# Kernel tuning notes

Hardware: AMD Instinct MI355X
Metric: run time of the kernel (lower is better)

The kernel has to match this reference:

```python
import jax, jax.numpy as jnp
import numpy as np

D_IN, D_SAE, T, L, K = 2304, 2048, 4, 6, 128
B = 32


def setup_inputs() -> dict:
    key = jax.random.key(0)
    kx, ke, kd = jax.random.split(key, 3)
    x = jax.random.normal(kx, (B, T, L, D_IN), dtype=jnp.float32)
    W_enc = jax.random.normal(ke, (T, L, D_IN, D_SAE), dtype=jnp.float32) / np.sqrt(D_IN).astype(np.float32)
    W_dec = jax.random.normal(kd, (T, L, D_SAE, D_IN), dtype=jnp.float32) / np.sqrt(D_SAE).astype(np.float32)
    b_enc = jnp.zeros((D_SAE,), dtype=jnp.float32)
    b_dec = jnp.zeros((T, L, D_IN), dtype=jnp.float32)
    return {"x": x, "W_enc": W_enc, "W_dec": W_dec, "b_enc": b_enc, "b_dec": b_dec}


def reference(x, W_enc, W_dec, b_enc, b_dec):
    # encode: per-(t,l) matmul, pre: (B, T, L, d_sae)
    pre = jnp.einsum('btld,tlds->btls', x, W_enc) + b_enc
    Bn = pre.shape[0]
    pre_flat = pre.reshape(Bn, T * L * D_SAE)
    # global TopK over the whole (T, L, d_sae) latent grid
    v, idx = jax.lax.top_k(pre_flat, K)
    z_flat = jnp.zeros_like(pre_flat).at[jnp.arange(Bn)[:, None], idx].set(jax.nn.relu(v))
    z = z_flat.reshape(Bn, T, L, D_SAE)
    # decode: per-(t,l) matmul
    x_hat = jnp.einsum('btls,tlsd->btld', z, W_dec) + b_dec
    loss = jnp.mean(jnp.sum(jnp.square(x_hat - x), axis=-1))
    return (loss, x_hat, z)
```

## Files before the change

### kernel.cpp

```cpp
#include <hip/hip_runtime.h>

#define D_IN   2304
#define D_SAE  2048
#define TL     24
#define BATCH  32
#define K_TOP  128
#define NLAT   (TL * D_SAE)
#define NBIN   8192
#define CAP    2048
#define KSPLIT 4
#define KS     (D_IN / KSPLIT)
#define BK     16
#define NCH    (KS / BK)

__device__ __forceinline__ void async_cp16(const float* g, float* l) {
    __builtin_amdgcn_global_load_lds(
        (const __attribute__((address_space(1))) unsigned int*)g,
        (__attribute__((address_space(3))) unsigned int*)l, 16, 0, 0);
}

__global__ __launch_bounds__(256, 3) void enc_kernel(const float* __restrict__ x,
                                                     const float* __restrict__ W,
                                                     float* __restrict__ part) {
    __shared__ float w_s[2][BK][256];
    __shared__ float x_s[2][BATCH][BK];

    const int tid  = threadIdx.x;
    const int lane = tid & 63;
    const int wv   = tid >> 6;
    const int cg   = tid & 63;
    const int tl   = blockIdx.y;
    const int ks   = blockIdx.z;

    const float* Wbase = W + ((size_t)(tl * D_IN + ks * KS)) * D_SAE + blockIdx.x * 256;

#define STAGE(buf, ch)                                                          \
    do {                                                                        \
        const float* Wc = Wbase + (size_t)((ch) * BK) * D_SAE;                  \
        _Pragma("unroll")                                                       \
        for (int j = 0; j < 4; ++j)                                             \
            async_cp16(Wc + (size_t)(wv * 4 + j) * D_SAE + lane * 4,            \
                       &w_s[buf][wv * 4 + j][0]);                               \
        _Pragma("unroll")                                                       \
        for (int p = 0; p < 2; ++p) {                                           \
            int f = p * 256 + lane * 4;      \
            int xb = f >> 4, xk = f & 15;                                       \
            async_cp16(x + ((size_t)(xb * TL + tl)) * D_IN + ks * KS            \
                         + (ch) * BK + xk,                                      \
                       &x_s[buf][0][0] + p * 256);                              \
        }                                                                       \
    } while (0)

    float4 acc[8];
#pragma unroll
    for (int j = 0; j < 8; ++j) acc[j] = make_float4(0.f, 0.f, 0.f, 0.f);

    STAGE(0, 0);

    int cur = 0;
    for (int ch = 0; ch < NCH; ++ch) {
        if (ch + 1 < NCH) {
            STAGE(cur ^ 1, ch + 1);
            asm volatile("s_waitcnt vmcnt(6)" ::: "memory");
        } else {
            asm volatile("s_waitcnt vmcnt(0)" ::: "memory");
        }
        asm volatile("s_barrier" ::: "memory");

        const float(*ws)[256] = w_s[cur];
        const float(*xs)[BK]  = x_s[cur];
#pragma unroll
        for (int k = 0; k < BK; ++k) {
            float4 w4 = *(const float4*)&ws[k][cg * 4];
#pragma unroll
            for (int j = 0; j < 8; ++j) {
                float xv = xs[wv * 8 + j][k];
                acc[j].x = fmaf(xv, w4.x, acc[j].x);
                acc[j].y = fmaf(xv, w4.y, acc[j].y);
                acc[j].z = fmaf(xv, w4.z, acc[j].z);
                acc[j].w = fmaf(xv, w4.w, acc[j].w);
            }
        }
        asm volatile("s_barrier" ::: "memory");
        cur ^= 1;
    }
#undef STAGE

    float* pp = part + ((size_t)ks * BATCH + wv * 8) * NLAT
              + (size_t)tl * D_SAE + blockIdx.x * 256 + cg * 4;
#pragma unroll
    for (int j = 0; j < 8; ++j)
        *(float4*)&pp[(size_t)j * NLAT] = acc[j];
}

__global__ void reduce_kernel(const float* __restrict__ part,
                              const float* __restrict__ b_enc,
                              float* __restrict__ pre) {
    int i = (blockIdx.x * blockDim.x + threadIdx.x) * 4;
    const size_t S = (size_t)BATCH * NLAT;
    float4 v = *(const float4*)&part[i];
    float4 v1 = *(const float4*)&part[i + S];
    float4 v2 = *(const float4*)&part[i + 2 * S];
    float4 v3 = *(const float4*)&part[i + 3 * S];
    float4 bb = *(const float4*)&b_enc[i & (D_SAE - 1)];
    v.x += v1.x + v2.x + v3.x + bb.x;
    v.y += v1.y + v2.y + v3.y + bb.y;
    v.z += v1.z + v2.z + v3.z + bb.z;
    v.w += v1.w + v2.w + v3.w + bb.w;
    *(float4*)&pre[i] = v;
}

__global__ __launch_bounds__(256) void topk_kernel(const float* __restrict__ pre,
                                                   int* __restrict__ sel_idx,
                                                   float* __restrict__ sel_val,
                                                   float* __restrict__ z,
                                                   float* __restrict__ loss) {
    const int b   = blockIdx.x;
    const int tid = threadIdx.x;
    __shared__ unsigned hist[NBIN];
    __shared__ unsigned cand_key[CAP];
    __shared__ int      cand_idx[CAP];
    __shared__ unsigned tsum[256];
    __shared__ unsigned suf[256];
    __shared__ int s_T, s_hi, s_ccnt, s_sel;

    const float* row  = pre + (size_t)b * NLAT;
    float*       zrow = z   + (size_t)b * NLAT;
    for (int i = tid; i < NBIN; i += 256) hist[i] = 0;
    if (tid == 0) { s_ccnt = 0; s_sel = 0; if (b == 0) *loss = 0.f; }
    __syncthreads();

    for (int i = 4 * tid; i < NLAT; i += 1024) {
        float4 v = *(const float4*)&row[i];
#pragma unroll
        for (int j = 0; j < 4; j++) {
            unsigned u   = __float_as_uint(((const float*)&v)[j]);
            unsigned key = u ^ ((u >> 31) ? 0xFFFFFFFFu : 0x80000000u);
            atomicAdd(&hist[key >> 19], 1u);
        }
    }
    __syncthreads();

    unsigned local = 0;
    const int base = tid * (NBIN / 256);
    for (int j = 0; j < NBIN / 256; j++) local += hist[base + j];
    tsum[tid] = local;
    __syncthreads();
    if (tid == 0) {
        unsigned run = 0;
        for (int t = 255; t >= 0; t--) { suf[t] = run; run += tsum[t]; }
    }
    __syncthreads();
    if (suf[tid] < K_TOP && suf[tid] + tsum[tid] >= K_TOP) {
        unsigned c = suf[tid];
        for (int j = NBIN / 256 - 1; j >= 0; j--) {
            int bin = base + j;
            if (c + hist[bin] >= K_TOP) { s_T = bin; s_hi = (int)c; break; }
            c += hist[bin];
        }
    }
    __syncthreads();

    const int T = s_T;
    for (int i = 4 * tid; i < NLAT; i += 1024) {
        float4 v = *(const float4*)&row[i];
#pragma unroll
        for (int j = 0; j < 4; j++) {
            float f      = ((const float*)&v)[j];
            unsigned u   = __float_as_uint(f);
            unsigned key = u ^ ((u >> 31) ? 0xFFFFFFFFu : 0x80000000u);
            int bin      = (int)(key >> 19);
            float rl     = fmaxf(f, 0.f);
            float zval   = 0.f;
            if (bin > T) {
                int p = atomicAdd(&s_sel, 1);
                sel_idx[b * K_TOP + p] = i + j;
                sel_val[b * K_TOP + p] = rl;
                zval = rl;
            } else if (bin == T) {
                int p = atomicAdd(&s_ccnt, 1);
                if (p < CAP) { cand_key[p] = key; cand_idx[p] = i + j; }
            }
            zrow[i + j] = zval;
        }
    }
    __syncthreads();

    const int need = K_TOP - s_hi;
    const int nc   = min(s_ccnt, CAP);
    for (int c = tid; c < nc; c += 256) {
        unsigned kc = cand_key[c]; int ic = cand_idx[c];
        int rank = 0;
        for (int j = 0; j < nc; j++) {
            unsigned kj = cand_key[j]; int ij = cand_idx[j];
            rank += (kj > kc) || (kj == kc && ij < ic);
        }
        if (rank < need) {
            int p = atomicAdd(&s_sel, 1);
            float rl = fmaxf(row[ic], 0.f);
            sel_idx[b * K_TOP + p] = ic;
            sel_val[b * K_TOP + p] = rl;
            zrow[ic] = rl;
        }
    }
}

__global__ __launch_bounds__(256) void dec_kernel(const float* __restrict__ Wd,
                                                  const float* __restrict__ b_dec,
                                                  const float* __restrict__ x,
                                                  const int* __restrict__ sel_idx,
                                                  const float* __restrict__ sel_val,
                                                  float* __restrict__ xhat,
                                                  float* __restrict__ loss) {
    const int tl = blockIdx.x, b = blockIdx.y, tid = threadIdx.x;
    float acc[9];
#pragma unroll
    for (int r = 0; r < 9; r++) acc[r] = b_dec[tl * D_IN + tid + r * 256];

    __shared__ int   s_idx[K_TOP];
    __shared__ float s_val[K_TOP];
    if (tid < K_TOP) { s_idx[tid] = sel_idx[b * K_TOP + tid];
                       s_val[tid] = sel_val[b * K_TOP + tid]; }
    __syncthreads();

    for (int j = 0; j < K_TOP; j++) {
        int f = s_idx[j];
        if ((f >> 11) == tl) {
            float v = s_val[j];
            const float* wrow = Wd + (size_t)f * D_IN;
#pragma unroll
            for (int r = 0; r < 9; r++)
                acc[r] = fmaf(v, wrow[tid + r * 256], acc[r]);
        }
    }

    const float* xr = x    + ((size_t)b * TL + tl) * D_IN;
    float*       xo = xhat + ((size_t)b * TL + tl) * D_IN;
    float lsum = 0.f;
#pragma unroll
    for (int r = 0; r < 9; r++) {
        float d = acc[r] - xr[tid + r * 256];
        xo[tid + r * 256] = acc[r];
        lsum += d * d;
    }
    __shared__ float red[256];
    red[tid] = lsum; __syncthreads();
    for (int s = 128; s > 0; s >>= 1) {
        if (tid < s) red[tid] += red[tid + s];
        __syncthreads();
    }
    if (tid == 0) atomicAdd(loss, red[0] * (1.0f / (BATCH * TL)));
}

extern "C" void kernel_launch(void* const* d_in, const int* in_sizes, int n_in,
                              void* d_out, int out_size, void* d_ws, size_t ws_size,
                              hipStream_t stream) {
    const float* x     = (const float*)d_in[0];
    const float* W_enc = (const float*)d_in[1];
    const float* W_dec = (const float*)d_in[2];
    const float* b_enc = (const float*)d_in[3];
    const float* b_dec = (const float*)d_in[4];

    float* out  = (float*)d_out;
    float* loss = out;
    float* xhat = out + 1;
    float* z    = out + 1 + (size_t)BATCH * TL * D_IN;

    const size_t S = (size_t)BATCH * NLAT;
    float* part    = (float*)d_ws;
    float* pre     = part + (size_t)KSPLIT * S;
    int*   sel_idx = (int*)(pre + S);
    float* sel_val = (float*)(sel_idx + BATCH * K_TOP);

    enc_kernel<<<dim3(8, TL, KSPLIT), 256, 0, stream>>>(x, W_enc, part);
    reduce_kernel<<<(int)(S / 1024), 256, 0, stream>>>(part, b_enc, pre);
    topk_kernel<<<BATCH, 256, 0, stream>>>(pre, sel_idx, sel_val, z, loss);
    dec_kernel<<<dim3(TL, BATCH), 256, 0, stream>>>(W_dec, b_dec, x, sel_idx, sel_val,
                                                    xhat, loss);
}
```

Measured before the change: 196.2 us.

## Widen encoder tile to 512 columns, double K-split, vectorize x reads

The encoder GEMM block now covers 512 SAE columns, with two float4 accumulator sets per thread instead of one. It uses KSPLIT=8 and BK=8 and reads x from shared memory as float4 across four k values. The point is to raise the ratio of arithmetic to LDS traffic and keep the grid size the same (4x24x8 blocks). In exchange, the partial-sum buffer and reduce traffic double, register pressure grows (64 accumulator floats), and the workspace must be large enough for 8 partials.

```diff
diff --git a/kernel.cpp b/kernel.cpp
--- a/kernel.cpp
+++ b/kernel.cpp
@@ -8,9 +8,9 @@
 #define NLAT   (TL * D_SAE)
 #define NBIN   8192
 #define CAP    2048
-#define KSPLIT 4
+#define KSPLIT 8
 #define KS     (D_IN / KSPLIT)
-#define BK     16
+#define BK     8
 #define NCH    (KS / BK)
 
 __device__ __forceinline__ void async_cp16(const float* g, float* l) {
@@ -22,38 +22,38 @@
 __global__ __launch_bounds__(256, 3) void enc_kernel(const float* __restrict__ x,
                                                      const float* __restrict__ W,
                                                      float* __restrict__ part) {
-    __shared__ float w_s[2][BK][256];
+    __shared__ float w_s[2][BK][512];
     __shared__ float x_s[2][BATCH][BK];
 
     const int tid  = threadIdx.x;
     const int lane = tid & 63;
     const int wv   = tid >> 6;
-    const int cg   = tid & 63;
     const int tl   = blockIdx.y;
     const int ks   = blockIdx.z;
-
-    const float* Wbase = W + ((size_t)(tl * D_IN + ks * KS)) * D_SAE + blockIdx.x * 256;
+    const int col0 = blockIdx.x * 512;
+
+    const float* Wbase = W + ((size_t)(tl * D_IN + ks * KS)) * D_SAE + col0;
+    const float* xsrc = x + ((size_t)((lane >> 1) * TL + tl)) * D_IN
+                      + ks * KS + (lane & 1) * 4;
 
 #define STAGE(buf, ch)                                                          \
     do {                                                                        \
         const float* Wc = Wbase + (size_t)((ch) * BK) * D_SAE;                  \
         _Pragma("unroll")                                                       \
-        for (int j = 0; j < 4; ++j)                                             \
-            async_cp16(Wc + (size_t)(wv * 4 + j) * D_SAE + lane * 4,            \
-                       &w_s[buf][wv * 4 + j][0]);                               \
-        _Pragma("unroll")                                                       \
-        for (int p = 0; p < 2; ++p) {                                           \
-            int f = p * 256 + lane * 4;      \
-            int xb = f >> 4, xk = f & 15;                                       \
-            async_cp16(x + ((size_t)(xb * TL + tl)) * D_IN + ks * KS            \
-                         + (ch) * BK + xk,                                      \
-                       &x_s[buf][0][0] + p * 256);                              \
+        for (int j = 0; j < 2; ++j) {                                           \
+            int r = wv * 2 + j;                                                 \
+            async_cp16(Wc + (size_t)r * D_SAE + lane * 4,       &w_s[buf][r][0]);   \
+            async_cp16(Wc + (size_t)r * D_SAE + 256 + lane * 4, &w_s[buf][r][256]); \
         }                                                                       \
+        async_cp16(xsrc + (ch) * BK, &x_s[buf][0][0]);                          \
     } while (0)
 
-    float4 acc[8];
-#pragma unroll
-    for (int j = 0; j < 8; ++j) acc[j] = make_float4(0.f, 0.f, 0.f, 0.f);
+    float4 accA[8], accB[8];
+#pragma unroll
+    for (int j = 0; j < 8; ++j) {
+        accA[j] = make_float4(0.f, 0.f, 0.f, 0.f);
+        accB[j] = make_float4(0.f, 0.f, 0.f, 0.f);
+    }
 
     STAGE(0, 0);
 
@@ -61,24 +61,37 @@
     for (int ch = 0; ch < NCH; ++ch) {
         if (ch + 1 < NCH) {
             STAGE(cur ^ 1, ch + 1);
-            asm volatile("s_waitcnt vmcnt(6)" ::: "memory");
+            asm volatile("s_waitcnt vmcnt(5)" ::: "memory");
         } else {
             asm volatile("s_waitcnt vmcnt(0)" ::: "memory");
         }
         asm volatile("s_barrier" ::: "memory");
 
-        const float(*ws)[256] = w_s[cur];
+        const float(*ws)[512] = w_s[cur];
         const float(*xs)[BK]  = x_s[cur];
 #pragma unroll
-        for (int k = 0; k < BK; ++k) {
-            float4 w4 = *(const float4*)&ws[k][cg * 4];
-#pragma unroll
-            for (int j = 0; j < 8; ++j) {
-                float xv = xs[wv * 8 + j][k];
-                acc[j].x = fmaf(xv, w4.x, acc[j].x);
-                acc[j].y = fmaf(xv, w4.y, acc[j].y);
-                acc[j].z = fmaf(xv, w4.z, acc[j].z);
-                acc[j].w = fmaf(xv, w4.w, acc[j].w);
+        for (int g = 0; g < 2; ++g) {
+            float4 wA[4], wB[4];
+#pragma unroll
+            for (int k = 0; k < 4; ++k) {
+                wA[k] = *(const float4*)&ws[g * 4 + k][lane * 4];
+                wB[k] = *(const float4*)&ws[g * 4 + k][256 + lane * 4];
+            }
+#pragma unroll
+            for (int b = 0; b < 8; ++b) {
+                float4 xv = *(const float4*)&xs[wv * 8 + b][g * 4];
+                const float* xf = (const float*)&xv;
+#pragma unroll
+                for (int k = 0; k < 4; ++k) {
+                    accA[b].x = fmaf(xf[k], wA[k].x, accA[b].x);
+                    accA[b].y = fmaf(xf[k], wA[k].y, accA[b].y);
+                    accA[b].z = fmaf(xf[k], wA[k].z, accA[b].z);
+                    accA[b].w = fmaf(xf[k], wA[k].w, accA[b].w);
+                    accB[b].x = fmaf(xf[k], wB[k].x, accB[b].x);
+                    accB[b].y = fmaf(xf[k], wB[k].y, accB[b].y);
+                    accB[b].z = fmaf(xf[k], wB[k].z, accB[b].z);
+                    accB[b].w = fmaf(xf[k], wB[k].w, accB[b].w);
+                }
             }
         }
         asm volatile("s_barrier" ::: "memory");
@@ -87,10 +100,12 @@
 #undef STAGE
 
     float* pp = part + ((size_t)ks * BATCH + wv * 8) * NLAT
-              + (size_t)tl * D_SAE + blockIdx.x * 256 + cg * 4;
-#pragma unroll
-    for (int j = 0; j < 8; ++j)
-        *(float4*)&pp[(size_t)j * NLAT] = acc[j];
+              + (size_t)tl * D_SAE + col0 + lane * 4;
+#pragma unroll
+    for (int j = 0; j < 8; ++j) {
+        *(float4*)&pp[(size_t)j * NLAT]       = accA[j];
+        *(float4*)&pp[(size_t)j * NLAT + 256] = accB[j];
+    }
 }
 
 __global__ void reduce_kernel(const float* __restrict__ part,
@@ -98,15 +113,12 @@
                               float* __restrict__ pre) {
     int i = (blockIdx.x * blockDim.x + threadIdx.x) * 4;
     const size_t S = (size_t)BATCH * NLAT;
-    float4 v = *(const float4*)&part[i];
-    float4 v1 = *(const float4*)&part[i + S];
-    float4 v2 = *(const float4*)&part[i + 2 * S];
-    float4 v3 = *(const float4*)&part[i + 3 * S];
-    float4 bb = *(const float4*)&b_enc[i & (D_SAE - 1)];
-    v.x += v1.x + v2.x + v3.x + bb.x;
-    v.y += v1.y + v2.y + v3.y + bb.y;
-    v.z += v1.z + v2.z + v3.z + bb.z;
-    v.w += v1.w + v2.w + v3.w + bb.w;
+    float4 v = *(const float4*)&b_enc[i & (D_SAE - 1)];
+#pragma unroll
+    for (int s = 0; s < KSPLIT; s++) {
+        float4 p = *(const float4*)&part[i + s * S];
+        v.x += p.x; v.y += p.y; v.z += p.z; v.w += p.w;
+    }
     *(float4*)&pre[i] = v;
 }
 
@@ -272,7 +284,7 @@
     int*   sel_idx = (int*)(pre + S);
     float* sel_val = (float*)(sel_idx + BATCH * K_TOP);
 
-    enc_kernel<<<dim3(8, TL, KSPLIT), 256, 0, stream>>>(x, W_enc, part);
+    enc_kernel<<<dim3(4, TL, KSPLIT), 256, 0, stream>>>(x, W_enc, part);
     reduce_kernel<<<(int)(S / 1024), 256, 0, stream>>>(part, b_enc, pre);
     topk_kernel<<<BATCH, 256, 0, stream>>>(pre, sel_idx, sel_val, z, loss);
     dec_kernel<<<dim3(TL, BATCH), 256, 0, stream>>>(W_dec, b_dec, x, sel_idx, sel_val,
```

After: 199.9 us. Within noise of the previous version (+1.9%).

## Pre-transpose x into k-major layout for vectorized encoder LDS reads

Applied to the files above, without the earlier changes.

Adds a transpose kernel that writes x as [tl][k][batch], so the encoder stages x tiles with contiguous 16-byte async copies and reads them as float4 broadcasts instead of scalar strided LDS loads. The encoder's pipeline wait moves to the end of each chunk (full vmcnt(0) drain), and its occupancy hint is raised to 4 blocks per CU. This costs an extra launch plus an extra pass over x, and the end-of-chunk full drain may expose more load latency.

```diff
diff --git a/kernel.cpp b/kernel.cpp
--- a/kernel.cpp
+++ b/kernel.cpp
@@ -19,20 +19,37 @@
         (__attribute__((address_space(3))) unsigned int*)l, 16, 0, 0);
 }
 
-__global__ __launch_bounds__(256, 3) void enc_kernel(const float* __restrict__ x,
+__global__ __launch_bounds__(256) void xT_kernel(const float* __restrict__ x,
+                                                 float* __restrict__ xT) {
+    __shared__ float ts[32][257];
+    const int tl = blockIdx.y, k0 = blockIdx.x * 256, tid = threadIdx.x;
+#pragma unroll 4
+    for (int r = 0; r < 32; ++r)
+        ts[r][tid] = x[((size_t)(r * TL + tl)) * D_IN + k0 + tid];
+    __syncthreads();
+    const int bb = tid & 31, kq = tid >> 5;
+#pragma unroll 4
+    for (int jj = 0; jj < 32; ++jj) {
+        int kk = kq + jj * 8;
+        xT[((size_t)tl * D_IN + k0 + kk) * 32 + bb] = ts[bb][kk];
+    }
+}
+
+__global__ __launch_bounds__(256, 4) void enc_kernel(const float* __restrict__ xT,
                                                      const float* __restrict__ W,
                                                      float* __restrict__ part) {
     __shared__ float w_s[2][BK][256];
-    __shared__ float x_s[2][BATCH][BK];
+    __shared__ float x_s[2][BK][32];
 
     const int tid  = threadIdx.x;
     const int lane = tid & 63;
     const int wv   = tid >> 6;
-    const int cg   = tid & 63;
     const int tl   = blockIdx.y;
     const int ks   = blockIdx.z;
-
-    const float* Wbase = W + ((size_t)(tl * D_IN + ks * KS)) * D_SAE + blockIdx.x * 256;
+    const int col0 = blockIdx.x * 256;
+
+    const float* Wbase = W + ((size_t)(tl * D_IN + ks * KS)) * D_SAE + col0;
+    const float* xbase = xT + ((size_t)(tl * D_IN + ks * KS)) * 32;
 
 #define STAGE(buf, ch)                                                          \
     do {                                                                        \
@@ -41,14 +58,8 @@
         for (int j = 0; j < 4; ++j)                                             \
             async_cp16(Wc + (size_t)(wv * 4 + j) * D_SAE + lane * 4,            \
                        &w_s[buf][wv * 4 + j][0]);                               \
-        _Pragma("unroll")                                                       \
-        for (int p = 0; p < 2; ++p) {                                           \
-            int f = p * 256 + lane * 4;      \
-            int xb = f >> 4, xk = f & 15;                                       \
-            async_cp16(x + ((size_t)(xb * TL + tl)) * D_IN + ks * KS            \
-                         + (ch) * BK + xk,                                      \
-                       &x_s[buf][0][0] + p * 256);                              \
-        }                                                                       \
+        async_cp16(xbase + (ch) * (BK * 32) + lane * 4,       &x_s[buf][0][0]); \
+        async_cp16(xbase + (ch) * (BK * 32) + 256 + lane * 4, &x_s[buf][8][0]); \
     } while (0)
 
     float4 acc[8];
@@ -56,38 +67,42 @@
     for (int j = 0; j < 8; ++j) acc[j] = make_float4(0.f, 0.f, 0.f, 0.f);
 
     STAGE(0, 0);
+    asm volatile("s_waitcnt vmcnt(0)" ::: "memory");
+    __builtin_amdgcn_s_barrier();
 
     int cur = 0;
     for (int ch = 0; ch < NCH; ++ch) {
-        if (ch + 1 < NCH) {
-            STAGE(cur ^ 1, ch + 1);
-            asm volatile("s_waitcnt vmcnt(6)" ::: "memory");
-        } else {
-            asm volatile("s_waitcnt vmcnt(0)" ::: "memory");
-        }
-        asm volatile("s_barrier" ::: "memory");
+        if (ch + 1 < NCH) STAGE(cur ^ 1, ch + 1);
 
         const float(*ws)[256] = w_s[cur];
-        const float(*xs)[BK]  = x_s[cur];
+        const float(*xs)[32]  = x_s[cur];
 #pragma unroll
         for (int k = 0; k < BK; ++k) {
-            float4 w4 = *(const float4*)&ws[k][cg * 4];
-#pragma unroll
-            for (int j = 0; j < 8; ++j) {
-                float xv = xs[wv * 8 + j][k];
-                acc[j].x = fmaf(xv, w4.x, acc[j].x);
-                acc[j].y = fmaf(xv, w4.y, acc[j].y);
-                acc[j].z = fmaf(xv, w4.z, acc[j].z);
-                acc[j].w = fmaf(xv, w4.w, acc[j].w);
+            float4 w4  = *(const float4*)&ws[k][lane * 4];
+            float4 xlo = *(const float4*)&xs[k][wv * 8];
+            float4 xhi = *(const float4*)&xs[k][wv * 8 + 4];
+            const float* xl = (const float*)&xlo;
+            const float* xh = (const float*)&xhi;
+#pragma unroll
+            for (int j = 0; j < 4; ++j) {
+                acc[j].x     = fmaf(xl[j], w4.x, acc[j].x);
+                acc[j].y     = fmaf(xl[j], w4.y, acc[j].y);
+                acc[j].z     = fmaf(xl[j], w4.z, acc[j].z);
+                acc[j].w     = fmaf(xl[j], w4.w, acc[j].w);
+                acc[j + 4].x = fmaf(xh[j], w4.x, acc[j + 4].x);
+                acc[j + 4].y = fmaf(xh[j], w4.y, acc[j + 4].y);
+                acc[j + 4].z = fmaf(xh[j], w4.z, acc[j + 4].z);
+                acc[j + 4].w = fmaf(xh[j], w4.w, acc[j + 4].w);
             }
         }
-        asm volatile("s_barrier" ::: "memory");
+        asm volatile("s_waitcnt vmcnt(0)" ::: "memory");
+        __builtin_amdgcn_s_barrier();
         cur ^= 1;
     }
 #undef STAGE
 
     float* pp = part + ((size_t)ks * BATCH + wv * 8) * NLAT
-              + (size_t)tl * D_SAE + blockIdx.x * 256 + cg * 4;
+              + (size_t)tl * D_SAE + col0 + lane * 4;
 #pragma unroll
     for (int j = 0; j < 8; ++j)
         *(float4*)&pp[(size_t)j * NLAT] = acc[j];
@@ -98,15 +113,12 @@
                               float* __restrict__ pre) {
     int i = (blockIdx.x * blockDim.x + threadIdx.x) * 4;
     const size_t S = (size_t)BATCH * NLAT;
-    float4 v = *(const float4*)&part[i];
-    float4 v1 = *(const float4*)&part[i + S];
-    float4 v2 = *(const float4*)&part[i + 2 * S];
-    float4 v3 = *(const float4*)&part[i + 3 * S];
-    float4 bb = *(const float4*)&b_enc[i & (D_SAE - 1)];
-    v.x += v1.x + v2.x + v3.x + bb.x;
-    v.y += v1.y + v2.y + v3.y + bb.y;
-    v.z += v1.z + v2.z + v3.z + bb.z;
-    v.w += v1.w + v2.w + v3.w + bb.w;
+    float4 v = *(const float4*)&b_enc[i & (D_SAE - 1)];
+#pragma unroll
+    for (int s = 0; s < KSPLIT; s++) {
+        float4 p = *(const float4*)&part[i + s * S];
+        v.x += p.x; v.y += p.y; v.z += p.z; v.w += p.w;
+    }
     *(float4*)&pre[i] = v;
 }
 
@@ -269,10 +281,12 @@
     const size_t S = (size_t)BATCH * NLAT;
     float* part    = (float*)d_ws;
     float* pre     = part + (size_t)KSPLIT * S;
-    int*   sel_idx = (int*)(pre + S);
+    float* xT      = pre + S;
+    int*   sel_idx = (int*)(xT + (size_t)TL * D_IN * BATCH);
     float* sel_val = (float*)(sel_idx + BATCH * K_TOP);
 
-    enc_kernel<<<dim3(8, TL, KSPLIT), 256, 0, stream>>>(x, W_enc, part);
+    xT_kernel<<<dim3(D_IN / 256, TL), 256, 0, stream>>>(x, xT);
+    enc_kernel<<<dim3(8, TL, KSPLIT), 256, 0, stream>>>(xT, W_enc, part);
     reduce_kernel<<<(int)(S / 1024), 256, 0, stream>>>(part, b_enc, pre);
     topk_kernel<<<BATCH, 256, 0, stream>>>(pre, sel_idx, sel_val, z, loss);
     dec_kernel<<<dim3(TL, BATCH), 256, 0, stream>>>(W_dec, b_dec, x, sel_idx, sel_val,
```

New measurement: 204.3 us. +4.2%, slower.
